# Kernel tuning notes

Measured on AMD Instinct MI355X. Metric: run time of the kernel, lower is better.

The kernel has to match this reference:

```python
import jax, jax.numpy as jnp
import numpy as np


def setup_inputs() -> dict:
    key = jax.random.key(0)
    k1, k2, k3 = jax.random.split(key, 3)
    N, F, E, H = 50000, 256, 800000, 4
    P = F // H + 1            # proj = 65
    dk = P * H                # 260
    x = jax.random.normal(k1, (N, F), dtype=jnp.float32)
    W = jax.random.normal(k2, (2 * dk, F), dtype=jnp.float32) * 0.02
    b = jnp.zeros((2 * dk,), dtype=jnp.float32)
    edge_index = jax.random.randint(k3, (2, E), 0, N, dtype=jnp.int32)
    return {"x": x, "edge_index": edge_index, "W": W, "b": b, "num_heads": H}


def reference(x, edge_index, W, b, num_heads):
    # x: [N, F]; W: [2*dk, F] with dk = P*num_heads; edge_index: [2, E]
    N = x.shape[0]
    P = W.shape[0] // (2 * num_heads)
    qk = x @ W.T + b                                   # [N, 2*dk]
    qk = qk.reshape(N, num_heads, 2 * P)               # 'L (h hdim) -> L h hdim'
    q, k = qk[..., :P], qk[..., P:]                    # split=2 outer -> q then k, each [N, H, P]
    src, dst = edge_index[0], edge_index[1]
    # per-edge dot product per head (NB: original never applies self.scale)
    scores = jnp.einsum('ehp,ehp->eh', q[src], k[dst])  # [E, H]
    # sparse softmax over dim=2 (columns) i.e. segment-softmax grouped by row index per head
    smax = jax.ops.segment_max(scores, src, num_segments=N)  # [N, H]
    ex = jnp.exp(scores - smax[src])                         # [E, H]
    denom = jax.ops.segment_sum(ex, src, num_segments=N)     # [N, H]
    attn = ex / denom[src]                                   # [E, H]
    # torch.sparse.sum(attn, dim=0) / num_heads -> mean over heads per edge
    vals = attn.mean(axis=1)                                 # [E]
    return vals
```

## Files before the change

### kernel.cpp

```cpp
#include <hip/hip_runtime.h>
#include <hip/hip_bf16.h>

#define K_DIM 256
#define RQ    512
#define NPAD  640
#define GBM 128
#define GBN 128
#define GBK 32
#define EPITCH 152
#define NBK   104
#define CBLK  256
#define SBAND 12512
#define DBAND 25024

typedef unsigned short u16;
using short8  = __attribute__((ext_vector_type(8))) short;
using ushort8 = __attribute__((ext_vector_type(8))) unsigned short;
using f32x4   = __attribute__((ext_vector_type(4))) float;
using f32x2   = __attribute__((ext_vector_type(2))) float;

__device__ __forceinline__ float asf(unsigned u) {
  union { unsigned i; float f; } x; x.i = u; return x.f;
}
__device__ __forceinline__ u16 f2b(float f) {
  __hip_bfloat16 h = __float2bfloat16(f); return *(u16*)&h;
}

__device__ __forceinline__ int bucket_of(int s, int d) {
  int sband = s / SBAND;
  int dband = d / DBAND;
  int ssub  = (s - sband * SBAND) >> 10;
  return ((sband << 1) | dband) * 13 + ssub;
}

__device__ __forceinline__ int map2(int p) {
  if (p < 256) return (p >> 6) * 130 + (p & 63);
  if (p < 512) { int q = p - 256; return (q >> 6) * 130 + 65 + (q & 63); }
  if (p < 516) return (p - 512) * 130 + 64;
  if (p < 520) return (p - 516) * 130 + 129;
  return -1;
}

__global__ void __launch_bounds__(256) prep(
    const float* __restrict__ x, const float* __restrict__ W,
    const float* __restrict__ bv, const int* __restrict__ ei,
    u16* __restrict__ xb, u16* __restrict__ wb,
    float* __restrict__ bias, float* __restrict__ zbase,
    int* __restrict__ counts,
    int M, int Mpad, int E, int per, int xblocks, int wblocks, int zblocks)
{
  __shared__ int h[NBK];
  const int blk = blockIdx.x, tid = threadIdx.x;
  if (blk < xblocks) {
    int idx = blk * 256 + tid;
    int total = Mpad * (K_DIM / 8);
    if (idx >= total) return;
    int row = idx / (K_DIM / 8);
    ushort8 o;
    if (row < M) {
      const float* s = x + (size_t)idx * 8;
      float4 a = *(const float4*)s;
      float4 b = *(const float4*)(s + 4);
      o[0] = f2b(a.x); o[1] = f2b(a.y); o[2] = f2b(a.z); o[3] = f2b(a.w);
      o[4] = f2b(b.x); o[5] = f2b(b.y); o[6] = f2b(b.z); o[7] = f2b(b.w);
    } else {
      #pragma unroll
      for (int j = 0; j < 8; ++j) o[j] = 0;
    }
    *(ushort8*)(xb + (size_t)idx * 8) = o;
  } else if (blk < xblocks + wblocks) {
    int idx = (blk - xblocks) * 256 + tid;
    int total = NPAD * (K_DIM / 8);
    if (idx >= total) return;
    int p  = idx / (K_DIM / 8);
    int kc = (idx % (K_DIM / 8)) * 8;
    int c  = map2(p);
    ushort8 o;
    if (c >= 0) {
      const float* s = W + (size_t)c * K_DIM + kc;
      float4 a = *(const float4*)s;
      float4 v = *(const float4*)(s + 4);
      o[0] = f2b(a.x); o[1] = f2b(a.y); o[2] = f2b(a.z); o[3] = f2b(a.w);
      o[4] = f2b(v.x); o[5] = f2b(v.y); o[6] = f2b(v.z); o[7] = f2b(v.w);
    } else {
      #pragma unroll
      for (int j = 0; j < 8; ++j) o[j] = 0;
    }
    *(ushort8*)(wb + (size_t)idx * 8) = o;
    if (kc == 0) bias[p] = (c >= 0) ? bv[c] : 0.f;
  } else if (blk < xblocks + wblocks + zblocks) {
    int i = (blk - xblocks - wblocks) * 256 + tid;
    if (i < M * 4) zbase[i] = 0.f;
  } else {
    int cb = blk - xblocks - wblocks - zblocks;
    if (tid < NBK) h[tid] = 0;
    __syncthreads();
    int start = cb * per, end = min(start + per, E);
    for (int i = start + tid; i < end; i += 256)
      atomicAdd(&h[bucket_of(ei[i], ei[E + i])], 1);
    __syncthreads();
    if (tid < NBK) counts[tid * CBLK + cb] = h[tid];
  }
}

__global__ void __launch_bounds__(256) gemm_mfma(
    const u16* __restrict__ xb, const u16* __restrict__ wb,
    const float* __restrict__ bias, u16* __restrict__ qkb,
    u16* __restrict__ tl, int M)
{
  __shared__ u16 smem[GBM * EPITCH];
  const int tid  = threadIdx.x;
  const int wave = tid >> 6, lane = tid & 63;
  const int l15 = lane & 15, lhi = lane >> 4;
  const int row0 = blockIdx.x * GBM, p0 = blockIdx.y * GBN;
  const int wr = (wave >> 1) * 64, wc = (wave & 1) * 64;

  f32x4 acc[4][4];
  #pragma unroll
  for (int m = 0; m < 4; ++m)
    #pragma unroll
    for (int n = 0; n < 4; ++n) acc[m][n] = (f32x4){0.f, 0.f, 0.f, 0.f};

#define STAGE(b, k0) do {                                                     \
    u16* As_ = smem + (b) * 8192;                                             \
    u16* Bs_ = As_ + 4096;                                                    \
    _Pragma("unroll")                                                         \
    for (int i_ = 0; i_ < 2; ++i_) {                                          \
      int f_ = wave * 128 + i_ * 64 + lane;                                   \
      int r_ = f_ >> 2, c_ = f_ & 3;                                          \
      const u16* gA = xb + (size_t)(row0 + r_) * K_DIM + (k0) + c_ * 8;       \
      __builtin_amdgcn_global_load_lds(                                       \
          (const __attribute__((address_space(1))) void*)gA,                  \
          (__attribute__((address_space(3))) void*)(As_ + (wave*128 + i_*64)*8), \
          16, 0, 0);                                                          \
      const u16* gB = wb + (size_t)(p0 + r_) * K_DIM + (k0) + c_ * 8;         \
      __builtin_amdgcn_global_load_lds(                                       \
          (const __attribute__((address_space(1))) void*)gB,                  \
          (__attribute__((address_space(3))) void*)(Bs_ + (wave*128 + i_*64)*8), \
          16, 0, 0);                                                          \
    }                                                                         \
  } while (0)

  STAGE(0, 0);
  asm volatile("s_waitcnt vmcnt(0)" ::: "memory");
  __syncthreads();

  #pragma unroll
  for (int t = 0; t < K_DIM / GBK; ++t) {
    if (t < K_DIM / GBK - 1) STAGE((t + 1) & 1, (t + 1) * GBK);
    const u16* As = smem + (t & 1) * 8192;
    const u16* Bs = As + 4096;
    short8 af[4], bf[4];
    #pragma unroll
    for (int m = 0; m < 4; ++m)
      af[m] = *(const short8*)(As + (size_t)(wr + m * 16 + l15) * GBK + lhi * 8);
    #pragma unroll
    for (int n = 0; n < 4; ++n)
      bf[n] = *(const short8*)(Bs + (size_t)(wc + n * 16 + l15) * GBK + lhi * 8);
    #pragma unroll
    for (int m = 0; m < 4; ++m)
      #pragma unroll
      for (int n = 0; n < 4; ++n)
        acc[m][n] = __builtin_amdgcn_mfma_f32_16x16x32_bf16(af[m], bf[n], acc[m][n], 0, 0, 0);
    if (t < K_DIM / GBK - 1) {
      asm volatile("s_waitcnt vmcnt(0)" ::: "memory");
      __syncthreads();
    }
  }
#undef STAGE

  __syncthreads();

  #pragma unroll
  for (int n = 0; n < 4; ++n) {
    int col = wc + n * 16 + l15;
    float bvv = bias[p0 + col];
    #pragma unroll
    for (int m = 0; m < 4; ++m) {
      #pragma unroll
      for (int r = 0; r < 4; ++r) {
        int row = wr + m * 16 + lhi * 4 + r;
        smem[row * EPITCH + col] = f2b(acc[m][n][r] + bvv);
      }
    }
  }
  __syncthreads();

  if (p0 < 512) {
    #pragma unroll
    for (int it = 0; it < 8; ++it) {
      int row  = wave * 32 + it * 4 + lhi;
      int grow = row0 + row;
      uint4 v = *(const uint4*)(smem + row * EPITCH + l15 * 8);
      if (grow < M)
        *(uint4*)(qkb + (size_t)grow * RQ + p0 + l15 * 8) = v;
    }
  } else {
    #pragma unroll
    for (int it = 0; it < 8; ++it) {
      int row  = wave * 32 + it * 4 + lhi;
      int grow = row0 + row;
      if (l15 == 0 && grow < M) {
        uint4 v = *(const uint4*)(smem + row * EPITCH);
        *(uint4*)(tl + (size_t)grow * 8) = v;
      }
    }
  }
}

__global__ void __launch_bounds__(1024) scan_k(int* __restrict__ counts)
{
  __shared__ int tot[NBK], base[NBK];
  const int tid = threadIdx.x, wv = tid >> 6, ln = tid & 63;
  for (int k = wv; k < NBK; k += 16) {
    int sum = 0;
    #pragma unroll
    for (int c = 0; c < CBLK / 64; ++c) sum += counts[k * CBLK + c * 64 + ln];
    #pragma unroll
    for (int off = 1; off < 64; off <<= 1) sum += __shfl_xor(sum, off);
    if (ln == 0) tot[k] = sum;
  }
  __syncthreads();
  if (tid == 0) {
    int run = 0;
    for (int k = 0; k < NBK; ++k) { base[k] = run; run += tot[k]; }
  }
  __syncthreads();
  for (int k = wv; k < NBK; k += 16) {
    int carry = base[k];
    #pragma unroll
    for (int c = 0; c < CBLK / 64; ++c) {
      int v = counts[k * CBLK + c * 64 + ln];
      int inc = v;
      #pragma unroll
      for (int off = 1; off < 64; off <<= 1) {
        int u = __shfl_up(inc, off);
        if (ln >= off) inc += u;
      }
      int last = __shfl(inc, 63);
      counts[k * CBLK + c * 64 + ln] = carry + inc - v;
      carry += last;
    }
  }
}

__global__ void __launch_bounds__(256) scatter2_k(
    const int* __restrict__ ei, const int* __restrict__ offs,
    uint2* __restrict__ sorted, int E, int per)
{
  __shared__ int cur[NBK];
  const int tid = threadIdx.x, blk = blockIdx.x;
  if (tid < NBK) cur[tid] = offs[tid * CBLK + blk];
  __syncthreads();
  int start = blk * per, end = min(start + per, E);
  for (int i = start + tid; i < end; i += 256) {
    int s = ei[i], d = ei[E + i];
    int pos = atomicAdd(&cur[bucket_of(s, d)], 1);
    sorted[pos] = make_uint2(((unsigned)s << 16) | (unsigned)d, (unsigned)i);
  }
}

__global__ void __launch_bounds__(256) edge_pass(
    const u16* __restrict__ qkb, const u16* __restrict__ tl,
    const uint2* __restrict__ sorted,
    float* __restrict__ exb, float* __restrict__ denom, int E)
{
  const int tid  = threadIdx.x;
  const int wave = tid >> 6, lane = tid & 63;
  const int g = lane >> 3;
  const int l = lane & 7;

  const int nwg = gridDim.x;
  const int q8 = nwg >> 3, r8 = nwg & 7;
  const int xcd = blockIdx.x & 7, bix = blockIdx.x >> 3;
  const int swz = (xcd < r8) ? (xcd * (q8 + 1) + bix)
                             : (r8 * (q8 + 1) + (xcd - r8) * q8 + bix);

  const int slot = swz * 32 + wave * 8 + g;
  const bool valid = slot < E;
  uint2 tr = sorted[valid ? slot : 0];
  const int src = tr.x >> 16, dst = tr.x & 0xffff;
  const int e = tr.y;

  const u16* qrow = qkb + ((size_t)src * RQ) + l * 32;
  const u16* krow = qkb + ((size_t)dst * RQ) + 256 + l * 32;

  int2 ti = make_int2(0, 0);
  if (l < 2) {
    const u16* tp = tl + (size_t)(l ? dst : src) * 8 + (l ? 4 : 0);
    ti = *(const int2*)tp;
  }

  f32x2 a2 = {0.f, 0.f};
  #pragma unroll
  for (int c = 0; c < 4; ++c) {
    uint4 qv = *(const uint4*)(qrow + c * 8);
    uint4 kv = *(const uint4*)(krow + c * 8);
    const unsigned* qd = (const unsigned*)&qv;
    const unsigned* kd = (const unsigned*)&kv;
    #pragma unroll
    for (int j = 0; j < 4; ++j) {
      f32x2 qa = { asf(qd[j] << 16), asf(qd[j] & 0xffff0000u) };
      f32x2 ka = { asf(kd[j] << 16), asf(kd[j] & 0xffff0000u) };
      a2 += qa * ka;
    }
  }
  float s = a2[0] + a2[1];
  s += __shfl_xor(s, 1);

  const int h = l >> 1;
  int idxA = ((g << 3) | (l & 1)) << 2;
  int w01 = __builtin_amdgcn_ds_bpermute(idxA, ti.x);
  int w23 = __builtin_amdgcn_ds_bpermute(idxA, ti.y);
  unsigned wsel = (h & 2) ? (unsigned)w23 : (unsigned)w01;
  float tv = (h & 1) ? asf(wsel & 0xffff0000u) : asf(wsel << 16);
  float to = __shfl_xor(tv, 1);
  s = fmaf(tv, to, s);

  float ev = __expf(s);
  if (valid && (l & 1) == 0) {
    exb[(size_t)e * 4 + h] = ev;
    unsafeAtomicAdd(&denom[(size_t)src * 4 + h], ev);
  }
}

__global__ void __launch_bounds__(256) finalize_k(
    const float* __restrict__ exb, const float* __restrict__ denom,
    const int* __restrict__ ei, float* __restrict__ out, int E)
{
  int e = blockIdx.x * 256 + threadIdx.x;
  if (e >= E) return;
  int src = ei[e];
  float4 ev = *(const float4*)(exb + (size_t)e * 4);
  float4 dv = *(const float4*)(denom + (size_t)src * 4);
  out[e] = 0.25f * (ev.x / dv.x + ev.y / dv.y + ev.z / dv.z + ev.w / dv.w);
}

extern "C" void kernel_launch(void* const* d_in, const int* in_sizes, int n_in,
                              void* d_out, int out_size, void* d_ws, size_t ws_size,
                              hipStream_t stream)
{
  const float* x  = (const float*)d_in[0];
  const int*   ei = (const int*)d_in[1];
  const float* W  = (const float*)d_in[2];
  const float* b  = (const float*)d_in[3];

  const int F = in_sizes[2] / in_sizes[3];
  const int M = in_sizes[0] / F;
  const int E = in_sizes[1] / 2;

  const int mblocks = (M + GBM - 1) / GBM;
  const int Mpad    = mblocks * GBM;

  u16* xb  = (u16*)d_ws;
  u16* wb  = xb + (size_t)Mpad * K_DIM;
  u16* qkb = wb + (size_t)NPAD * K_DIM;
  u16* tl  = qkb + (size_t)M * RQ;
  float* bias  = (float*)(tl + (size_t)M * 8);
  float* exb   = bias + NPAD;
  float* denom = exb + (size_t)E * 4;
  int*   counts = (int*)(denom + (size_t)M * 4);
  uint2* sorted = (uint2*)(counts + NBK * CBLK);

  const int xblocks = (Mpad * (K_DIM / 8) + 255) / 256;
  const int wblocks = (NPAD * (K_DIM / 8) + 255) / 256;
  const int zblocks = (M * 4 + 255) / 256;
  const int per     = (E + CBLK - 1) / CBLK;
  hipLaunchKernelGGL(prep, dim3(xblocks + wblocks + zblocks + CBLK), dim3(256), 0,
                     stream, x, W, b, ei, xb, wb, bias, denom, counts,
                     M, Mpad, E, per, xblocks, wblocks, zblocks);

  hipLaunchKernelGGL(scan_k, dim3(1), dim3(1024), 0, stream, counts);

  dim3 gg(mblocks, NPAD / GBN);
  hipLaunchKernelGGL(gemm_mfma, gg, dim3(256), 0, stream, xb, wb, bias, qkb, tl, M);

  hipLaunchKernelGGL(scatter2_k, dim3(CBLK), dim3(256), 0, stream,
                     ei, counts, sorted, E, per);

  int eblocks = (E + 31) / 32;
  hipLaunchKernelGGL(edge_pass, dim3(eblocks), dim3(256), 0, stream,
                     qkb, tl, sorted, exb, denom, E);

  hipLaunchKernelGGL(finalize_k, dim3((E + 255) / 256), dim3(256), 0, stream,
                     exb, denom, ei, (float*)d_out, E);
}
```

Before: 176.8 us.

## Use 2D src/dst tiled edge buckets, flat scan, and fp16 exp buffer

Edges are now bucketed by 2048-node src and dst sub-tiles inside each band, interleaved in a Morton-like order, so consecutive edges touch both q rows and k rows that sit close together. This aims to improve cache locality of the gathers in the edge pass. The bucket count grows to 1024 with 128 counting blocks, and the scan is rewritten as a single flat block-wide prefix sum. The per-edge exp values are stored as fp16 to halve that write and read traffic, at some cost in precision and a risk of overflow for large scores.

```diff
diff --git a/kernel.cpp b/kernel.cpp
--- a/kernel.cpp
+++ b/kernel.cpp
@@ -8,8 +8,8 @@
 #define GBN 128
 #define GBK 32
 #define EPITCH 152
-#define NBK   104
-#define CBLK  256
+#define NBK   1024
+#define CBLK  128
 #define SBAND 12512
 #define DBAND 25024
 
@@ -25,12 +25,17 @@
 __device__ __forceinline__ u16 f2b(float f) {
   __hip_bfloat16 h = __float2bfloat16(f); return *(u16*)&h;
 }
+__device__ __forceinline__ u16 f2h(float f) { _Float16 h = (_Float16)f; return *(u16*)&h; }
+__device__ __forceinline__ float h2f(u16 u) { _Float16 h = *(_Float16*)&u; return (float)h; }
 
 __device__ __forceinline__ int bucket_of(int s, int d) {
   int sband = s / SBAND;
   int dband = d / DBAND;
-  int ssub  = (s - sband * SBAND) >> 10;
-  return ((sband << 1) | dband) * 13 + ssub;
+  int ss = (s - sband * SBAND) >> 11;
+  int dd = (d - dband * DBAND) >> 11;
+  int m = ((ss & 4) << 4) | ((dd & 8) << 2) | ((ss & 2) << 3)
+        | ((dd & 4) << 1) | ((ss & 1) << 2) | (dd & 3);
+  return (((sband << 1) | dband) << 7) | m;
 }
 
 __device__ __forceinline__ int map2(int p) {
@@ -93,13 +98,13 @@
     if (i < M * 4) zbase[i] = 0.f;
   } else {
     int cb = blk - xblocks - wblocks - zblocks;
-    if (tid < NBK) h[tid] = 0;
+    for (int i = tid; i < NBK; i += 256) h[i] = 0;
     __syncthreads();
     int start = cb * per, end = min(start + per, E);
     for (int i = start + tid; i < end; i += 256)
       atomicAdd(&h[bucket_of(ei[i], ei[E + i])], 1);
     __syncthreads();
-    if (tid < NBK) counts[tid * CBLK + cb] = h[tid];
+    for (int i = tid; i < NBK; i += 256) counts[i * CBLK + cb] = h[i];
   }
 }
 
@@ -210,37 +215,34 @@
 
 __global__ void __launch_bounds__(1024) scan_k(int* __restrict__ counts)
 {
-  __shared__ int tot[NBK], base[NBK];
-  const int tid = threadIdx.x, wv = tid >> 6, ln = tid & 63;
-  for (int k = wv; k < NBK; k += 16) {
-    int sum = 0;
-    #pragma unroll
-    for (int c = 0; c < CBLK / 64; ++c) sum += counts[k * CBLK + c * 64 + ln];
-    #pragma unroll
-    for (int off = 1; off < 64; off <<= 1) sum += __shfl_xor(sum, off);
-    if (ln == 0) tot[k] = sum;
-  }
-  __syncthreads();
-  if (tid == 0) {
-    int run = 0;
-    for (int k = 0; k < NBK; ++k) { base[k] = run; run += tot[k]; }
-  }
-  __syncthreads();
-  for (int k = wv; k < NBK; k += 16) {
-    int carry = base[k];
-    #pragma unroll
-    for (int c = 0; c < CBLK / 64; ++c) {
-      int v = counts[k * CBLK + c * 64 + ln];
-      int inc = v;
-      #pragma unroll
-      for (int off = 1; off < 64; off <<= 1) {
-        int u = __shfl_up(inc, off);
-        if (ln >= off) inc += u;
-      }
-      int last = __shfl(inc, 63);
-      counts[k * CBLK + c * 64 + ln] = carry + inc - v;
-      carry += last;
-    }
+  __shared__ int wtot[16];
+  const int t = threadIdx.x, ln = t & 63, wv = t >> 6;
+  const int base_i = t * (NBK * CBLK / 1024);
+  int sum = 0;
+  for (int i = 0; i < NBK * CBLK / 1024; ++i) sum += counts[base_i + i];
+  int inc = sum;
+  #pragma unroll
+  for (int off = 1; off < 64; off <<= 1) {
+    int u = __shfl_up(inc, off);
+    if (ln >= off) inc += u;
+  }
+  if (ln == 63) wtot[wv] = inc;
+  __syncthreads();
+  if (wv == 0 && ln < 16) {
+    int v = wtot[ln], in2 = v;
+    #pragma unroll
+    for (int off = 1; off < 16; off <<= 1) {
+      int u = __shfl_up(in2, off);
+      if (ln >= off) in2 += u;
+    }
+    wtot[ln] = in2 - v;
+  }
+  __syncthreads();
+  int run = (inc - sum) + wtot[wv];
+  for (int i = 0; i < NBK * CBLK / 1024; ++i) {
+    int v = counts[base_i + i];
+    counts[base_i + i] = run;
+    run += v;
   }
 }
 
@@ -250,7 +252,7 @@
 {
   __shared__ int cur[NBK];
   const int tid = threadIdx.x, blk = blockIdx.x;
-  if (tid < NBK) cur[tid] = offs[tid * CBLK + blk];
+  for (int i = tid; i < NBK; i += 256) cur[i] = offs[i * CBLK + blk];
   __syncthreads();
   int start = blk * per, end = min(start + per, E);
   for (int i = start + tid; i < end; i += 256) {
@@ -263,7 +265,7 @@
 __global__ void __launch_bounds__(256) edge_pass(
     const u16* __restrict__ qkb, const u16* __restrict__ tl,
     const uint2* __restrict__ sorted,
-    float* __restrict__ exb, float* __restrict__ denom, int E)
+    u16* __restrict__ exh, float* __restrict__ denom, int E)
 {
   const int tid  = threadIdx.x;
   const int wave = tid >> 6, lane = tid & 63;
@@ -319,21 +321,22 @@
 
   float ev = __expf(s);
   if (valid && (l & 1) == 0) {
-    exb[(size_t)e * 4 + h] = ev;
+    exh[(size_t)e * 4 + h] = f2h(ev);
     unsafeAtomicAdd(&denom[(size_t)src * 4 + h], ev);
   }
 }
 
 __global__ void __launch_bounds__(256) finalize_k(
-    const float* __restrict__ exb, const float* __restrict__ denom,
+    const u16* __restrict__ exh, const float* __restrict__ denom,
     const int* __restrict__ ei, float* __restrict__ out, int E)
 {
   int e = blockIdx.x * 256 + threadIdx.x;
   if (e >= E) return;
   int src = ei[e];
-  float4 ev = *(const float4*)(exb + (size_t)e * 4);
+  ushort4 ev = *(const ushort4*)(exh + (size_t)e * 4);
   float4 dv = *(const float4*)(denom + (size_t)src * 4);
-  out[e] = 0.25f * (ev.x / dv.x + ev.y / dv.y + ev.z / dv.z + ev.w / dv.w);
+  out[e] = 0.25f * (h2f(ev.x) / dv.x + h2f(ev.y) / dv.y
+                  + h2f(ev.z) / dv.z + h2f(ev.w) / dv.w);
 }
 
 extern "C" void kernel_launch(void* const* d_in, const int* in_sizes, int n_in,
@@ -357,8 +360,8 @@
   u16* qkb = wb + (size_t)NPAD * K_DIM;
   u16* tl  = qkb + (size_t)M * RQ;
   float* bias  = (float*)(tl + (size_t)M * 8);
-  float* exb   = bias + NPAD;
-  float* denom = exb + (size_t)E * 4;
+  u16*   exh   = (u16*)(bias + NPAD);
+  float* denom = (float*)(exh + (size_t)E * 4);
   int*   counts = (int*)(denom + (size_t)M * 4);
   uint2* sorted = (uint2*)(counts + NBK * CBLK);
 
@@ -380,8 +383,8 @@
 
   int eblocks = (E + 31) / 32;
   hipLaunchKernelGGL(edge_pass, dim3(eblocks), dim3(256), 0, stream,
-                     qkb, tl, sorted, exb, denom, E);
+                     qkb, tl, sorted, exh, denom, E);
 
   hipLaunchKernelGGL(finalize_k, dim3((E + 255) / 256), dim3(256), 0, stream,
-                     exb, denom, ei, (float*)d_out, E);
-}
+                     exh, denom, ei, (float*)d_out, E);
+}
```

Measured after the change: 225.0 us. 27.3% more time.
